# Performance work log

Measured on AMD Instinct MI355X. Metric: run time of the kernel, lower is better.

## Reference

```python
import jax, jax.numpy as jnp
import numpy as np

DIM = 1024

def setup_inputs() -> dict:
    key = jax.random.key(0)
    k1, k2, k3, k4 = jax.random.split(key, 4)
    x = jax.random.normal(k1, (4, 2048, DIM), dtype=jnp.float32)
    # nn.Linear(dim, dim).weight tensors, shape [dim, dim]
    wk = jax.random.normal(k2, (DIM, DIM), dtype=jnp.float32) * 0.02
    wq = jax.random.normal(k3, (DIM, DIM), dtype=jnp.float32) * 0.02
    wv = jax.random.normal(k4, (DIM, DIM), dtype=jnp.float32) * 0.02
    return {"x": x, "wk": wk, "wq": wq, "wv": wv}

def reference(x, wk, wq, wv):
    B, N, d = x.shape
    scale = N ** -0.5
    # stochastic value weights: softmax over dim 0 of W_v, scaled, transposed
    wv_stoch = (jax.nn.softmax(wv, axis=0) * (1.0 / d)).T
    query = x @ wq                       # [B, N, d]
    key_t = jnp.swapaxes(x @ wk, -1, -2) # [B, d, N]
    value = x @ wv_stoch                 # [B, N, d]
    scores = jnp.einsum('bnd,bdm->bnm', query, key_t) * scale  # [B, N, N]
    # softmax over dim=1 (column-wise, over queries) then subtract identity
    attn = jax.nn.softmax(scores, axis=1) - jnp.eye(N, dtype=x.dtype)
    return attn @ value
```

## Files before the change

### kernel.cpp

```cpp
#include <hip/hip_runtime.h>
#include <hip/hip_bf16.h>
#include <hip/hip_fp8.h>
#include <cstdint>
#include <cmath>

typedef __bf16 bf16_t;
typedef __bf16 bf16x8 __attribute__((ext_vector_type(8)));
typedef __bf16 bf16x4 __attribute__((ext_vector_type(4)));
typedef float floatx4 __attribute__((ext_vector_type(4)));
typedef int   intx4  __attribute__((ext_vector_type(4)));
typedef int   intx8  __attribute__((ext_vector_type(8)));

#define MB ((size_t)1 << 20)

static __device__ __forceinline__ void async_load16(const void* g, void* l) {
    __builtin_amdgcn_global_load_lds(
        (const __attribute__((address_space(1))) uint32_t*)(uintptr_t)g,
        (__attribute__((address_space(3))) uint32_t*)(uint32_t)(uintptr_t)l,
        16, 0, 0);
}

static __device__ __forceinline__ uint8_t to_fp8(float v) {
    __hip_fp8_e4m3 h(v);
    return *reinterpret_cast<uint8_t*>(&h);
}


__global__ void prep_many(const float* __restrict__ x, uint8_t* __restrict__ x8,
                          float* __restrict__ Srow,
                          const float* __restrict__ wq, const float* __restrict__ wk,
                          uint8_t* __restrict__ wcat8, const float* __restrict__ wv,
                          float* __restrict__ part) {
    __shared__ float tile[32][33];
    __shared__ float wsum[4];
    const int bid = blockIdx.x, t = threadIdx.x;
    if (bid < 8192) {
        int i = bid * 256 + t;
        float4 v = ((const float4*)x)[i];
        uint32_t pk = (uint32_t)to_fp8(v.x) | ((uint32_t)to_fp8(v.y) << 8) |
                      ((uint32_t)to_fp8(v.z) << 16) | ((uint32_t)to_fp8(v.w) << 24);
        ((uint32_t*)x8)[i] = pk;
        float s = (v.x + v.y) + (v.z + v.w);
        #pragma unroll
        for (int d = 1; d < 64; d <<= 1) s += __shfl_xor(s, d);
        if ((t & 63) == 0) wsum[t >> 6] = s;
        __syncthreads();
        if (t == 0) Srow[bid] = (wsum[0] + wsum[1]) + (wsum[2] + wsum[3]);
    } else if (bid < 10240) {
        int b2 = bid - 8192;
        const float* W = (b2 >= 1024) ? wk : wq;
        uint8_t* outp = wcat8 + (size_t)(b2 >> 10) * 1024 * 1024;
        int b3 = b2 & 1023;
        int c0 = (b3 & 31) * 32, r0 = (b3 >> 5) * 32;
        int tx = t & 31, ty = t >> 5;
        #pragma unroll
        for (int i = 0; i < 4; i++)
            tile[ty + i * 8][tx] = W[(r0 + ty + i * 8) * 1024 + c0 + tx];
        __syncthreads();
        #pragma unroll
        for (int i = 0; i < 4; i++)
            outp[(long)(c0 + ty + i * 8) * 1024 + r0 + tx] = to_fp8(tile[tx][ty + i * 8]);
    } else {
        int b = bid - 10240;
        int d = (b & 3) * 256 + t;
        int g = b >> 2;
        float s = 0.f;
        #pragma unroll
        for (int i = 0; i < 16; i++) s += __expf(wv[(g * 16 + i) * 1024 + d]);
        part[g * 1024 + d] = s;
    }
}

__global__ void colsum_stage2(const float* __restrict__ part, float* __restrict__ cs) {
    int d = blockIdx.x * 256 + threadIdx.x;
    float s = 0.f;
    #pragma unroll 8
    for (int g = 0; g < 64; g++) s += part[g * 1024 + d];
    cs[d] = s;
}

__global__ void prep_delta(const float* __restrict__ wv, const float* __restrict__ cs,
                           uint8_t* __restrict__ delta8) {
    int idx = blockIdx.x * 256 + threadIdx.x;
    int d = idx & 1023;
    float r = __expf(wv[idx]) * 1024.0f / cs[d] - 1.0f;
    delta8[idx] = to_fp8(r * 16.0f);
}

__global__ void scale_transpose_vp(const bf16_t* __restrict__ vp,
                                   const float* __restrict__ Lpart,
                                   uint8_t* __restrict__ vpT) {
    __shared__ float tile[32][33];
    __shared__ float ls[32];
    int t = threadIdx.x;
    int tx = t & 31, ty = t >> 5;
    int e0 = blockIdx.x * 32;
    int m0 = blockIdx.y * 32;
    if (t < 32) {
        int m = m0 + t, z = m >> 11, ml = m & 2047;
        float s = 0.f;
        #pragma unroll
        for (int y = 0; y < 16; y++) s += Lpart[(z * 16 + y) * 2048 + ml];
        ls[t] = 1073741824.0f / s;
    }
    __syncthreads();
    #pragma unroll
    for (int i = 0; i < 4; i++) {
        int mr = ty + i * 8;
        tile[mr][tx] = (float)vp[(long)(m0 + mr) * 1024 + e0 + tx] * ls[mr];
    }
    __syncthreads();
    int b = m0 >> 11, ml = m0 & 2047;
    #pragma unroll
    for (int i = 0; i < 4; i++)
        vpT[((long)(b * 1024 + e0 + ty + i * 8)) * 2048 + ml + tx] = to_fp8(tile[tx][ty + i * 8]);
}

template <int EPI>
__global__ __launch_bounds__(256, 3) void gemm_nt_fp8(
    const uint8_t* __restrict__ A, const uint8_t* __restrict__ B, void* __restrict__ C,
    uint8_t* __restrict__ C1, bf16_t* __restrict__ Cv, const float* __restrict__ Srow,
    float* __restrict__ Lout, const bf16_t* __restrict__ Vp,
    int N, int K, long aBatch, long bBatch, long cBatch, float scaleExp)
{
    __shared__ __align__(16) uint8_t ldsA[128 * 128];
    __shared__ __align__(16) uint8_t ldsB[128 * 128];
    const int t = threadIdx.x;
    const int z = blockIdx.z;
    const uint8_t* Ab = A + (long)z * aBatch + (long)blockIdx.y * 128 * K;
    const uint8_t* Bb = B + (long)z * bBatch + (long)blockIdx.x * 128 * K;
    const int r  = t >> 3;
    const int cg = (t & 7) ^ (r & 7);
    const uint8_t* ag0 = Ab + (long)r * K + cg * 16;
    const uint8_t* bg0 = Bb + (long)r * K + cg * 16;
    uint8_t* la = ldsA + t * 16;
    uint8_t* lb = ldsB + t * 16;
    const int lane = t & 63, wave = t >> 6;
    const int wm = (wave >> 1) * 64, wn = (wave & 1) * 64;
    const int fr = lane & 15;
    const int q4 = lane >> 4;
    const int sw = fr & 7;

    floatx4 zero = {0.f, 0.f, 0.f, 0.f};
    floatx4 acc[4][4];
    #pragma unroll
    for (int i = 0; i < 4; i++)
        #pragma unroll
        for (int j = 0; j < 4; j++) acc[i][j] = zero;

    for (int k0 = 0; k0 < K; k0 += 128) {
        __syncthreads();
        #pragma unroll
        for (int i = 0; i < 4; i++) {
            async_load16(ag0 + (long)(32 * i) * K + k0, la + 4096 * i);
            async_load16(bg0 + (long)(32 * i) * K + k0, lb + 4096 * i);
        }
        __syncthreads();
        intx8 af[4], bfr[4];
        #pragma unroll
        for (int i = 0; i < 4; i++) {
            int row = wm + i * 16 + fr;
            intx4 lo = *(const intx4*)(ldsA + row * 128 + ((2 * q4) ^ sw) * 16);
            intx4 hi = *(const intx4*)(ldsA + row * 128 + ((2 * q4 + 1) ^ sw) * 16);
            af[i][0] = lo[0]; af[i][1] = lo[1]; af[i][2] = lo[2]; af[i][3] = lo[3];
            af[i][4] = hi[0]; af[i][5] = hi[1]; af[i][6] = hi[2]; af[i][7] = hi[3];
        }
        #pragma unroll
        for (int j = 0; j < 4; j++) {
            int row = wn + j * 16 + fr;
            intx4 lo = *(const intx4*)(ldsB + row * 128 + ((2 * q4) ^ sw) * 16);
            intx4 hi = *(const intx4*)(ldsB + row * 128 + ((2 * q4 + 1) ^ sw) * 16);
            bfr[j][0] = lo[0]; bfr[j][1] = lo[1]; bfr[j][2] = lo[2]; bfr[j][3] = lo[3];
            bfr[j][4] = hi[0]; bfr[j][5] = hi[1]; bfr[j][6] = hi[2]; bfr[j][7] = hi[3];
        }
        #pragma unroll
        for (int i = 0; i < 4; i++)
            #pragma unroll
            for (int j = 0; j < 4; j++)
                acc[i][j] = __builtin_amdgcn_mfma_scale_f32_16x16x128_f8f6f4(
                    af[i], bfr[j], acc[i][j], 0, 0,
                    0, 0x7f7f7f7f, 0, 0x7f7f7f7f);
    }

    const int rq = (lane >> 4) * 4;
    const long rowBase = (long)blockIdx.y * 128 + wm;
    const int colBase = blockIdx.x * 128 + wn;

    if constexpr (EPI == 0) {
        const int sel = blockIdx.x >> 3;
        const int cB = (blockIdx.x & 7) * 128 + wn;
        if (sel == 2) {
            const float c24 = 5.9604644775390625e-08f;
            const float c20 = 9.5367431640625e-07f;
            #pragma unroll
            for (int mi = 0; mi < 4; mi++)
                #pragma unroll
                for (int rr = 0; rr < 4; rr++) {
                    long row = rowBase + mi * 16 + rq + rr;
                    float sv = Srow[row] * c20;
                    #pragma unroll
                    for (int ni = 0; ni < 4; ni++)
                        Cv[row * 1024 + cB + ni * 16 + fr] =
                            (bf16_t)(acc[mi][ni][rr] * c24 + sv);
                }
        } else {
            uint8_t* Cb = sel ? C1 : (uint8_t*)C;
            #pragma unroll
            for (int mi = 0; mi < 4; mi++)
                #pragma unroll
                for (int rr = 0; rr < 4; rr++) {
                    long row = rowBase + mi * 16 + rq + rr;
                    #pragma unroll
                    for (int ni = 0; ni < 4; ni++)
                        Cb[row * 1024 + cB + ni * 16 + fr] = to_fp8(acc[mi][ni][rr]);
                }
        }
    } else if constexpr (EPI == 2) {
        uint8_t* Cb = (uint8_t*)C + (long)z * cBatch;
        float csum[4] = {0.f, 0.f, 0.f, 0.f};
        #pragma unroll
        for (int mi = 0; mi < 4; mi++)
            #pragma unroll
            for (int rr = 0; rr < 4; rr++) {
                long row = rowBase + mi * 16 + rq + rr;
                #pragma unroll
                for (int ni = 0; ni < 4; ni++) {
                    float p = __expf(acc[mi][ni][rr] * scaleExp);
                    Cb[row * N + colBase + ni * 16 + fr] = to_fp8(p);
                    csum[ni] += p;
                }
            }
        float red[4];
        #pragma unroll
        for (int ni = 0; ni < 4; ni++) {
            float v = csum[ni];
            v += __shfl_xor(v, 16);
            v += __shfl_xor(v, 32);
            red[ni] = v;
        }
        __syncthreads();
        float* lf = (float*)ldsA;
        #pragma unroll
        for (int ni = 0; ni < 4; ni++)
            if (lane < 16)
                lf[(wm >> 6) * 128 + wn + ni * 16 + lane] = red[ni];
        __syncthreads();
        if (t < 128) {
            float s = lf[t] + lf[128 + t];
            Lout[(long)(z * 16 + blockIdx.y) * 2048 + blockIdx.x * 128 + t] = s;
        }
    } else {
        float* Co = (float*)C + (long)z * cBatch;
        const bf16_t* Vb = Vp + (long)z * cBatch;
        const float inv230 = 9.313225746154785e-10f;
        #pragma unroll
        for (int mi = 0; mi < 4; mi++)
            #pragma unroll
            for (int rr = 0; rr < 4; rr++) {
                long row = rowBase + mi * 16 + rq + rr;
                #pragma unroll
                for (int ni = 0; ni < 4; ni++) {
                    int col = colBase + ni * 16 + fr;
                    Co[row * N + col] = acc[mi][ni][rr] * inv230 - (float)Vb[row * N + col];
                }
            }
    }
}


extern "C" void kernel_launch(void* const* d_in, const int* in_sizes, int n_in,
                              void* d_out, int out_size, void* d_ws, size_t ws_size,
                              hipStream_t stream) {
    const float* x  = (const float*)d_in[0];
    const float* wk = (const float*)d_in[1];
    const float* wq = (const float*)d_in[2];
    const float* wv = (const float*)d_in[3];
    float* out = (float*)d_out;

    char* ws = (char*)d_ws;
    uint8_t* x8     = (uint8_t*)(ws + 0);
    uint8_t* wcat8  = (uint8_t*)(ws + 8 * MB);
    uint8_t* delta8 = wcat8 + 2u * 1024 * 1024;
    uint8_t* P      = (uint8_t*)(ws + 0);
    float*   wvpart = (float*)(ws + 32 * MB);
    uint8_t* q8     = (uint8_t*)(ws + 32 * MB);
    uint8_t* vpT    = (uint8_t*)(ws + 32 * MB);
    uint8_t* k8     = (uint8_t*)(ws + 48 * MB);
    bf16_t*  vp     = (bf16_t*)(ws + 64 * MB);
    float*   cs     = (float*)(ws + 80 * MB);
    float*   Srow   = (float*)(ws + 80 * MB + 16 * 1024);
    float*   Lpart  = (float*)(ws + 80 * MB + 64 * 1024);

    const float scale = 0.022097086912079608f;

    prep_many<<<10496, 256, 0, stream>>>(x, x8, Srow, wq, wk, wcat8, wv, wvpart);
    colsum_stage2<<<4, 256, 0, stream>>>(wvpart, cs);
    prep_delta<<<4096, 256, 0, stream>>>(wv, cs, delta8);

    gemm_nt_fp8<0><<<dim3(24, 64, 1), 256, 0, stream>>>(x8, wcat8, q8,
        k8, vp, Srow, nullptr, nullptr, 1024, 1024, 0, 0, 0, 0.f);

    gemm_nt_fp8<2><<<dim3(16, 16, 4), 256, 0, stream>>>(q8, k8, P,
        nullptr, nullptr, nullptr, Lpart, nullptr, 2048, 1024,
        (long)2048 * 1024, (long)2048 * 1024, (long)2048 * 2048, scale);

    scale_transpose_vp<<<dim3(32, 256), 256, 0, stream>>>(vp, Lpart, vpT);

    gemm_nt_fp8<3><<<dim3(8, 16, 4), 256, 0, stream>>>(P, vpT, out,
        nullptr, nullptr, nullptr, nullptr, vp, 1024, 2048,
        (long)2048 * 2048, (long)1024 * 2048, (long)2048 * 1024, 0.f);
}
```

Measured before the change: 189.7 us.

## Swap GEMM grid axes, use exp2 in softmax epilogue, prereduce column sums

Swaps the block-index mapping in the FP8 GEMM so blockIdx.x walks the A row tiles and blockIdx.y the B column tiles, changing block dispatch order and L2 reuse of the B operand. Replaces __expf with the hardware exp2 builtin, folding log2(e) into the scale constant. Adds a small kernel that reduces the 16 partial column sums once, instead of each transpose block re-summing them. The extra launch adds a little overhead in exchange for less redundant work in the transpose.

```diff
diff --git a/kernel.cpp b/kernel.cpp
--- a/kernel.cpp
+++ b/kernel.cpp
@@ -87,8 +87,17 @@
     delta8[idx] = to_fp8(r * 16.0f);
 }
 
+__global__ void reduce_L(const float* __restrict__ Lpart, float* __restrict__ L) {
+    int i = blockIdx.x * 256 + threadIdx.x;
+    int z = i >> 11, col = i & 2047;
+    float s = 0.f;
+    #pragma unroll
+    for (int y = 0; y < 16; y++) s += Lpart[(z * 16 + y) * 2048 + col];
+    L[i] = s;
+}
+
 __global__ void scale_transpose_vp(const bf16_t* __restrict__ vp,
-                                   const float* __restrict__ Lpart,
+                                   const float* __restrict__ L,
                                    uint8_t* __restrict__ vpT) {
     __shared__ float tile[32][33];
     __shared__ float ls[32];
@@ -96,13 +105,7 @@
     int tx = t & 31, ty = t >> 5;
     int e0 = blockIdx.x * 32;
     int m0 = blockIdx.y * 32;
-    if (t < 32) {
-        int m = m0 + t, z = m >> 11, ml = m & 2047;
-        float s = 0.f;
-        #pragma unroll
-        for (int y = 0; y < 16; y++) s += Lpart[(z * 16 + y) * 2048 + ml];
-        ls[t] = 1073741824.0f / s;
-    }
+    if (t < 32) ls[t] = 1073741824.0f / L[m0 + t];
     __syncthreads();
     #pragma unroll
     for (int i = 0; i < 4; i++) {
@@ -127,8 +130,10 @@
     __shared__ __align__(16) uint8_t ldsB[128 * 128];
     const int t = threadIdx.x;
     const int z = blockIdx.z;
-    const uint8_t* Ab = A + (long)z * aBatch + (long)blockIdx.y * 128 * K;
-    const uint8_t* Bb = B + (long)z * bBatch + (long)blockIdx.x * 128 * K;
+    const int by = blockIdx.x;
+    const int bx = blockIdx.y;
+    const uint8_t* Ab = A + (long)z * aBatch + (long)by * 128 * K;
+    const uint8_t* Bb = B + (long)z * bBatch + (long)bx * 128 * K;
     const int r  = t >> 3;
     const int cg = (t & 7) ^ (r & 7);
     const uint8_t* ag0 = Ab + (long)r * K + cg * 16;
@@ -183,12 +188,12 @@
     }
 
     const int rq = (lane >> 4) * 4;
-    const long rowBase = (long)blockIdx.y * 128 + wm;
-    const int colBase = blockIdx.x * 128 + wn;
+    const long rowBase = (long)by * 128 + wm;
+    const int colBase = bx * 128 + wn;
 
     if constexpr (EPI == 0) {
-        const int sel = blockIdx.x >> 3;
-        const int cB = (blockIdx.x & 7) * 128 + wn;
+        const int sel = bx >> 3;
+        const int cB = (bx & 7) * 128 + wn;
         if (sel == 2) {
             const float c24 = 5.9604644775390625e-08f;
             const float c20 = 9.5367431640625e-07f;
@@ -225,7 +230,7 @@
                 long row = rowBase + mi * 16 + rq + rr;
                 #pragma unroll
                 for (int ni = 0; ni < 4; ni++) {
-                    float p = __expf(acc[mi][ni][rr] * scaleExp);
+                    float p = __builtin_amdgcn_exp2f(acc[mi][ni][rr] * scaleExp);
                     Cb[row * N + colBase + ni * 16 + fr] = to_fp8(p);
                     csum[ni] += p;
                 }
@@ -247,7 +252,7 @@
         __syncthreads();
         if (t < 128) {
             float s = lf[t] + lf[128 + t];
-            Lout[(long)(z * 16 + blockIdx.y) * 2048 + blockIdx.x * 128 + t] = s;
+            Lout[(long)(z * 16 + by) * 2048 + bx * 128 + t] = s;
         }
     } else {
         float* Co = (float*)C + (long)z * cBatch;
@@ -290,23 +295,26 @@
     float*   cs     = (float*)(ws + 80 * MB);
     float*   Srow   = (float*)(ws + 80 * MB + 16 * 1024);
     float*   Lpart  = (float*)(ws + 80 * MB + 64 * 1024);
-
-    const float scale = 0.022097086912079608f;
+    float*   L      = (float*)(ws + 80 * MB + 576 * 1024);
+
+    const float scaleExp2 = 0.0318793572f;
 
     prep_many<<<10496, 256, 0, stream>>>(x, x8, Srow, wq, wk, wcat8, wv, wvpart);
     colsum_stage2<<<4, 256, 0, stream>>>(wvpart, cs);
     prep_delta<<<4096, 256, 0, stream>>>(wv, cs, delta8);
 
-    gemm_nt_fp8<0><<<dim3(24, 64, 1), 256, 0, stream>>>(x8, wcat8, q8,
+    gemm_nt_fp8<0><<<dim3(64, 24, 1), 256, 0, stream>>>(x8, wcat8, q8,
         k8, vp, Srow, nullptr, nullptr, 1024, 1024, 0, 0, 0, 0.f);
 
     gemm_nt_fp8<2><<<dim3(16, 16, 4), 256, 0, stream>>>(q8, k8, P,
         nullptr, nullptr, nullptr, Lpart, nullptr, 2048, 1024,
-        (long)2048 * 1024, (long)2048 * 1024, (long)2048 * 2048, scale);
-
-    scale_transpose_vp<<<dim3(32, 256), 256, 0, stream>>>(vp, Lpart, vpT);
-
-    gemm_nt_fp8<3><<<dim3(8, 16, 4), 256, 0, stream>>>(P, vpT, out,
+        (long)2048 * 1024, (long)2048 * 1024, (long)2048 * 2048, scaleExp2);
+
+    reduce_L<<<32, 256, 0, stream>>>(Lpart, L);
+
+    scale_transpose_vp<<<dim3(32, 256), 256, 0, stream>>>(vp, L, vpT);
+
+    gemm_nt_fp8<3><<<dim3(16, 8, 4), 256, 0, stream>>>(P, vpT, out,
         nullptr, nullptr, nullptr, nullptr, vp, 1024, 2048,
         (long)2048 * 2048, (long)1024 * 2048, (long)2048 * 1024, 0.f);
 }
```

New measurement: 187.0 us. About the same (-1.4%).
